# Performance work log

Hardware: AMD Instinct MI355X
Metric: run time of the kernel (lower is better)

## Reference

```python
import jax, jax.numpy as jnp
import numpy as np

B, D, K, E = 256, 256, 1024, 16  # batch, dim_codes, book_size, embedding_dim
DECAY = 0.999
GAIN = 1.0 - DECAY
EPS = 1e-6


def setup_inputs() -> dict:
    key = jax.random.key(0)
    k1, k2 = jax.random.split(key)
    return {
        "cw_q": jax.random.normal(k1, (B, D * E), dtype=jnp.float32),
        "codebook": jax.random.normal(k2, (D, K, E), dtype=jnp.float32),
        "ema_counts": jnp.ones((D, K), dtype=jnp.float32),
    }


def reference(cw_q, codebook, ema_counts):
    batch = cw_q.shape[0]
    x = cw_q.reshape(batch, D, E)  # [B, D, E]

    x2 = jnp.sum(x * x, axis=-1)                       # [B, D]
    c2 = jnp.sum(codebook * codebook, axis=-1)         # [D, K]
    xc = jnp.einsum('bde,dke->bdk', x, codebook)       # [B, D, K]
    dist = x2[:, :, None] + c2[None, :, :] - 2.0 * xc

    idx = jnp.argmin(dist, axis=-1)                    # [B, D] int32

    # gather nearest code vector per (batch, dim_code)
    cw_embed = codebook[jnp.arange(D)[None, :], idx]   # [B, D, E]
    cw_embed = cw_embed.reshape(batch, D * E)

    one_hot_idx = jax.nn.one_hot(idx, K, dtype=cw_q.dtype)  # [B, D, K]

    # EMA update (training path): scatter-sum of assigned vectors per code
    update = jnp.einsum('bdk,bde->dke', one_hot_idx, x)      # [D, K, E]
    new_codebook = codebook * DECAY + GAIN * update / (ema_counts[:, :, None] + EPS)
    new_ema_counts = DECAY * ema_counts + GAIN * jnp.sum(one_hot_idx, axis=0)

    return cw_embed, one_hot_idx, new_codebook, new_ema_counts
```

## Files before the change

### kernel.cpp

```cpp
#include <hip/hip_runtime.h>
#include <float.h>

#define BB 256
#define DD 256
#define KK 1024
#define EE 16
#define DECAY 0.999f
#define GAIN  0.001f
#define EPS   1e-6f

#define OH_OFF   ((size_t)BB * DD * EE)
#define CB_OFF   (OH_OFF + (size_t)BB * DD * KK)
#define EMA_OFF  (CB_OFF + (size_t)DD * KK * EE)

__device__ __forceinline__ float dot16(const float4& a0, const float4& a1,
                                       const float4& a2, const float4& a3,
                                       const float4& b0, const float4& b1,
                                       const float4& b2, const float4& b3) {
  float s = a0.x * b0.x;
  s = fmaf(a0.y, b0.y, s); s = fmaf(a0.z, b0.z, s); s = fmaf(a0.w, b0.w, s);
  s = fmaf(a1.x, b1.x, s); s = fmaf(a1.y, b1.y, s); s = fmaf(a1.z, b1.z, s); s = fmaf(a1.w, b1.w, s);
  s = fmaf(a2.x, b2.x, s); s = fmaf(a2.y, b2.y, s); s = fmaf(a2.z, b2.z, s); s = fmaf(a2.w, b2.w, s);
  s = fmaf(a3.x, b3.x, s); s = fmaf(a3.y, b3.y, s); s = fmaf(a3.z, b3.z, s); s = fmaf(a3.w, b3.w, s);
  return s;
}

__global__ __launch_bounds__(256, 2) void vq_assign(
    const float* __restrict__ cw_q,
    const float* __restrict__ codebook,
    float* __restrict__ out,
    int* __restrict__ idx_ws)
{
  __shared__ float4 cb4s[KK * EE / 4];
  __shared__ float  c2s[KK];
  __shared__ float  pbest[4 * 128];
  __shared__ int    pidxs[4 * 128];

  const int t  = threadIdx.x;
  const int d  = blockIdx.x >> 1;
  const int hf = blockIdx.x & 1;
  const int w  = t >> 6;
  const int l  = t & 63;

  const int b0 = hf * 128 + l;
  const int b1 = b0 + 64;
  const float4* xr0 = (const float4*)cw_q + (size_t)b0 * (DD * EE / 4) + d * 4;
  const float4* xr1 = (const float4*)cw_q + (size_t)b1 * (DD * EE / 4) + d * 4;
  float4 xa0 = xr0[0], xb0 = xr0[1], xc0 = xr0[2], xd0 = xr0[3];
  float4 xa1 = xr1[0], xb1 = xr1[1], xc1 = xr1[2], xd1 = xr1[3];

  const float4* src4 = (const float4*)codebook + (size_t)d * (KK * EE / 4);
  #pragma unroll
  for (int i = 0; i < 16; ++i) {
    int i4 = i * 256 + t;
    float4 v = src4[i4];
    cb4s[i4] = v;
    float sq = v.x * v.x;
    sq = fmaf(v.y, v.y, sq);
    sq = fmaf(v.z, v.z, sq);
    sq = fmaf(v.w, v.w, sq);
    sq += __shfl_xor(sq, 1);
    sq += __shfl_xor(sq, 2);
    if ((t & 3) == 0) c2s[i4 >> 2] = sq;
  }
  __syncthreads();

  const float x2_0 = dot16(xa0, xb0, xc0, xd0, xa0, xb0, xc0, xd0);
  const float x2_1 = dot16(xa1, xb1, xc1, xd1, xa1, xb1, xc1, xd1);

  float best0 = FLT_MAX, best1 = FLT_MAX;
  int   bi0 = 0, bi1 = 0;
  const int kbase = w << 8;

  float2* zbase = (float2*)(out + OH_OFF + (size_t)(hf * 128) * (DD * KK)
                            + (size_t)d * KK + kbase) + l;

  #pragma unroll 2
  for (int s = 0; s < 256; ++s) {
    const int k = kbase + s;
    const float4* p = cb4s + (k << 2);
    float4 c0 = p[0], c1 = p[1], c2v = p[2], c3 = p[3];

    float dot0 = dot16(c0, c1, c2v, c3, xa0, xb0, xc0, xd0);
    float dot1 = dot16(c0, c1, c2v, c3, xa1, xb1, xc1, xd1);
    const float c2k = c2s[k];
    float d0 = fmaf(-2.f, dot0, x2_0 + c2k);
    float d1 = fmaf(-2.f, dot1, x2_1 + c2k);
    if (d0 < best0) { best0 = d0; bi0 = k; }
    if (d1 < best1) { best1 = d1; bi1 = k; }

    const int r  = s >> 1;
    const int hh = s & 1;
    zbase[(size_t)r * (DD * KK / 2) + hh * 64] = make_float2(0.f, 0.f);
  }

  pbest[w * 128 + l]      = best0;  pidxs[w * 128 + l]      = bi0;
  pbest[w * 128 + l + 64] = best1;  pidxs[w * 128 + l + 64] = bi1;
  __syncthreads();

  if (t < 128) {
    float bb = pbest[t];
    int   bi = pidxs[t];
    #pragma unroll
    for (int w2 = 1; w2 < 4; ++w2) {
      float e = pbest[w2 * 128 + t];
      int   ii = pidxs[w2 * 128 + t];
      if (e < bb) { bb = e; bi = ii; }
    }
    const int b = hf * 128 + t;

    float4* ce = (float4*)out + (size_t)b * (DD * EE / 4) + d * 4;
    const float4* cw = cb4s + (bi << 2);
    ce[0] = cw[0]; ce[1] = cw[1]; ce[2] = cw[2]; ce[3] = cw[3];

    out[OH_OFF + (size_t)b * (DD * KK) + (size_t)d * KK + bi] = 1.0f;

    idx_ws[d * BB + b] = bi;
  }
}

__global__ __launch_bounds__(256) void vq_update(
    const float* __restrict__ cw_q,
    const float* __restrict__ codebook,
    const float* __restrict__ ema,
    const int* __restrict__ idx_ws,
    float* __restrict__ out)
{
  __shared__ float upds[KK * EE];
  __shared__ float cnts[KK];
  __shared__ float esh[KK];
  __shared__ int   ish[BB];

  const int t = threadIdx.x;
  const int d = blockIdx.x;
  float4* upd4 = (float4*)upds;
  const float4 z4 = make_float4(0.f, 0.f, 0.f, 0.f);

  #pragma unroll
  for (int i = 0; i < 16; ++i) upd4[i * 256 + t] = z4;
  #pragma unroll
  for (int j = 0; j < 4; ++j) cnts[t + 256 * j] = 0.f;
  __syncthreads();

  {
    int kidx = idx_ws[d * BB + t];
    ish[t] = kidx;
    atomicAdd(&cnts[kidx], 1.0f);
  }
  __syncthreads();

  {
    const int e = t & 15;
    const int g = t >> 4;
    #pragma unroll
    for (int i = 0; i < 16; ++i) {
      int b = g * 16 + i;
      int k = ish[b];
      float xv = cw_q[(size_t)b * (DD * EE) + (size_t)d * EE + e];
      atomicAdd(&upds[k * EE + e], xv);
    }
  }
  __syncthreads();

  const float* emad = ema + (size_t)d * KK;
  float* out_ema    = out + EMA_OFF + (size_t)d * KK;
  #pragma unroll
  for (int j = 0; j < 4; ++j) {
    int k = t + 256 * j;
    float ev = emad[k];
    esh[k] = ev;
    out_ema[k] = DECAY * ev + GAIN * cnts[k];
  }
  __syncthreads();

  const float4* cb4 = (const float4*)codebook + (size_t)d * (KK * EE / 4);
  float4* ocb4      = (float4*)(out + CB_OFF) + (size_t)d * (KK * EE / 4);
  #pragma unroll
  for (int i = 0; i < 16; ++i) {
    int i4 = i * 256 + t;
    int k  = i4 >> 2;
    float4 c = cb4[i4];
    float4 u = upd4[i4];
    float inv = GAIN / (esh[k] + EPS);
    float4 r;
    r.x = DECAY * c.x + u.x * inv;
    r.y = DECAY * c.y + u.y * inv;
    r.z = DECAY * c.z + u.z * inv;
    r.w = DECAY * c.w + u.w * inv;
    ocb4[i4] = r;
  }
}

extern "C" void kernel_launch(void* const* d_in, const int* in_sizes, int n_in,
                              void* d_out, int out_size, void* d_ws, size_t ws_size,
                              hipStream_t stream) {
  const float* cw_q     = (const float*)d_in[0];
  const float* codebook = (const float*)d_in[1];
  const float* ema      = (const float*)d_in[2];
  float* out  = (float*)d_out;
  int* idx_ws = (int*)d_ws;
  (void)in_sizes; (void)n_in; (void)out_size; (void)ws_size;

  vq_assign<<<dim3(512), dim3(256), 0, stream>>>(cw_q, codebook, out, idx_ws);
  vq_update<<<dim3(256), dim3(256), 0, stream>>>(cw_q, codebook, ema, idx_ws, out);
}
```

Before: 327.5 us.

## Fuse VQ assignment and EMA update into one kernel per code dimension

Merges the assign and update kernels into a single 512-thread block per dimension. Each block now handles all 256 batch rows, four per thread, and keeps the codebook in LDS for the EMA update. This removes the index round-trip through workspace, the second codebook read and one launch. The one-hot zero fill moves from float2 to float4 stores over contiguous row segments. The cost is about 150 KB of LDS per block, which allows only one block per CU, and half as many blocks (256 instead of 512).

```diff
diff --git a/kernel.cpp b/kernel.cpp
--- a/kernel.cpp
+++ b/kernel.cpp
@@ -25,34 +25,35 @@
   return s;
 }
 
-__global__ __launch_bounds__(256, 2) void vq_assign(
+__global__ __launch_bounds__(512, 2) void vqvae_fused(
     const float* __restrict__ cw_q,
     const float* __restrict__ codebook,
-    float* __restrict__ out,
-    int* __restrict__ idx_ws)
+    const float* __restrict__ ema,
+    float* __restrict__ out)
 {
   __shared__ float4 cb4s[KK * EE / 4];
+  __shared__ float4 upd4s[KK * EE / 4];
   __shared__ float  c2s[KK];
-  __shared__ float  pbest[4 * 128];
-  __shared__ int    pidxs[4 * 128];
+  __shared__ float  cnts[KK];
+  __shared__ float  pbest[8 * 256];
+  __shared__ int    pidxs[8 * 256];
+  __shared__ int    ish[BB];
 
-  const int t  = threadIdx.x;
-  const int d  = blockIdx.x >> 1;
-  const int hf = blockIdx.x & 1;
-  const int w  = t >> 6;
-  const int l  = t & 63;
+  const int t = threadIdx.x;
+  const int d = blockIdx.x;
+  const int w = t >> 6;
+  const int l = t & 63;
+  const float4 z4 = make_float4(0.f, 0.f, 0.f, 0.f);
 
-  const int b0 = hf * 128 + l;
-  const int b1 = b0 + 64;
-  const float4* xr0 = (const float4*)cw_q + (size_t)b0 * (DD * EE / 4) + d * 4;
-  const float4* xr1 = (const float4*)cw_q + (size_t)b1 * (DD * EE / 4) + d * 4;
-  float4 xa0 = xr0[0], xb0 = xr0[1], xc0 = xr0[2], xd0 = xr0[3];
-  float4 xa1 = xr1[0], xb1 = xr1[1], xc1 = xr1[2], xd1 = xr1[3];
+  #pragma unroll
+  for (int j = 0; j < 2; ++j) cnts[t + 512 * j] = 0.f;
+  #pragma unroll
+  for (int i = 0; i < 8; ++i) upd4s[i * 512 + t] = z4;
 
   const float4* src4 = (const float4*)codebook + (size_t)d * (KK * EE / 4);
   #pragma unroll
-  for (int i = 0; i < 16; ++i) {
-    int i4 = i * 256 + t;
+  for (int i = 0; i < 8; ++i) {
+    int i4 = i * 512 + t;
     float4 v = src4[i4];
     cb4s[i4] = v;
     float sq = v.x * v.x;
@@ -63,131 +64,118 @@
     sq += __shfl_xor(sq, 2);
     if ((t & 3) == 0) c2s[i4 >> 2] = sq;
   }
+
+  float4 xv[4][4];
+  float  x2[4];
+  #pragma unroll
+  for (int j = 0; j < 4; ++j) {
+    const int b = l + 64 * j;
+    const float4* xr = (const float4*)cw_q + (size_t)b * (DD * EE / 4) + d * 4;
+    xv[j][0] = xr[0]; xv[j][1] = xr[1]; xv[j][2] = xr[2]; xv[j][3] = xr[3];
+  }
   __syncthreads();
 
-  const float x2_0 = dot16(xa0, xb0, xc0, xd0, xa0, xb0, xc0, xd0);
-  const float x2_1 = dot16(xa1, xb1, xc1, xd1, xa1, xb1, xc1, xd1);
+  #pragma unroll
+  for (int j = 0; j < 4; ++j)
+    x2[j] = dot16(xv[j][0], xv[j][1], xv[j][2], xv[j][3],
+                  xv[j][0], xv[j][1], xv[j][2], xv[j][3]);
 
-  float best0 = FLT_MAX, best1 = FLT_MAX;
-  int   bi0 = 0, bi1 = 0;
-  const int kbase = w << 8;
+  float best[4] = {FLT_MAX, FLT_MAX, FLT_MAX, FLT_MAX};
+  int   bi[4]   = {0, 0, 0, 0};
+  const int kbase = w << 7;
 
-  float2* zbase = (float2*)(out + OH_OFF + (size_t)(hf * 128) * (DD * KK)
-                            + (size_t)d * KK + kbase) + l;
+  float* ohp = out + OH_OFF;
+  float4* zb = (float4*)(ohp + (size_t)(w << 5) * (DD * KK) + (size_t)d * KK) + l;
 
   #pragma unroll 2
-  for (int s = 0; s < 256; ++s) {
+  for (int s = 0; s < 128; ++s) {
     const int k = kbase + s;
     const float4* p = cb4s + (k << 2);
     float4 c0 = p[0], c1 = p[1], c2v = p[2], c3 = p[3];
+    const float c2k = c2s[k];
 
-    float dot0 = dot16(c0, c1, c2v, c3, xa0, xb0, xc0, xd0);
-    float dot1 = dot16(c0, c1, c2v, c3, xa1, xb1, xc1, xd1);
-    const float c2k = c2s[k];
-    float d0 = fmaf(-2.f, dot0, x2_0 + c2k);
-    float d1 = fmaf(-2.f, dot1, x2_1 + c2k);
-    if (d0 < best0) { best0 = d0; bi0 = k; }
-    if (d1 < best1) { best1 = d1; bi1 = k; }
+    #pragma unroll
+    for (int j = 0; j < 4; ++j) {
+      float dj = dot16(c0, c1, c2v, c3, xv[j][0], xv[j][1], xv[j][2], xv[j][3]);
+      float dist = fmaf(-2.f, dj, x2[j] + c2k);
+      if (dist < best[j]) { best[j] = dist; bi[j] = k; }
+    }
 
-    const int r  = s >> 1;
-    const int hh = s & 1;
-    zbase[(size_t)r * (DD * KK / 2) + hh * 64] = make_float2(0.f, 0.f);
+    zb[(size_t)(s >> 2) * (DD * KK / 4) + (s & 3) * 64] = z4;
   }
 
-  pbest[w * 128 + l]      = best0;  pidxs[w * 128 + l]      = bi0;
-  pbest[w * 128 + l + 64] = best1;  pidxs[w * 128 + l + 64] = bi1;
+  #pragma unroll
+  for (int j = 0; j < 4; ++j) {
+    pbest[w * 256 + l + 64 * j] = best[j];
+    pidxs[w * 256 + l + 64 * j] = bi[j];
+  }
   __syncthreads();
 
-  if (t < 128) {
-    float bb = pbest[t];
-    int   bi = pidxs[t];
+  if (t < 256) {
+    const int b = t;
+    float bb = pbest[b];
+    int   bidx = pidxs[b];
     #pragma unroll
-    for (int w2 = 1; w2 < 4; ++w2) {
-      float e = pbest[w2 * 128 + t];
-      int   ii = pidxs[w2 * 128 + t];
-      if (e < bb) { bb = e; bi = ii; }
+    for (int w2 = 1; w2 < 8; ++w2) {
+      float e = pbest[w2 * 256 + b];
+      int   ii = pidxs[w2 * 256 + b];
+      if (e < bb) { bb = e; bidx = ii; }
     }
-    const int b = hf * 128 + t;
 
     float4* ce = (float4*)out + (size_t)b * (DD * EE / 4) + d * 4;
-    const float4* cw = cb4s + (bi << 2);
-    ce[0] = cw[0]; ce[1] = cw[1]; ce[2] = cw[2]; ce[3] = cw[3];
+    const float4* cwp = cb4s + (bidx << 2);
+    ce[0] = cwp[0]; ce[1] = cwp[1]; ce[2] = cwp[2]; ce[3] = cwp[3];
 
-    out[OH_OFF + (size_t)b * (DD * KK) + (size_t)d * KK + bi] = 1.0f;
+    ohp[(size_t)b * (DD * KK) + (size_t)d * KK + bidx] = 1.0f;
 
-    idx_ws[d * BB + b] = bi;
-  }
-}
-
-__global__ __launch_bounds__(256) void vq_update(
-    const float* __restrict__ cw_q,
-    const float* __restrict__ codebook,
-    const float* __restrict__ ema,
-    const int* __restrict__ idx_ws,
-    float* __restrict__ out)
-{
-  __shared__ float upds[KK * EE];
-  __shared__ float cnts[KK];
-  __shared__ float esh[KK];
-  __shared__ int   ish[BB];
-
-  const int t = threadIdx.x;
-  const int d = blockIdx.x;
-  float4* upd4 = (float4*)upds;
-  const float4 z4 = make_float4(0.f, 0.f, 0.f, 0.f);
-
-  #pragma unroll
-  for (int i = 0; i < 16; ++i) upd4[i * 256 + t] = z4;
-  #pragma unroll
-  for (int j = 0; j < 4; ++j) cnts[t + 256 * j] = 0.f;
-  __syncthreads();
-
-  {
-    int kidx = idx_ws[d * BB + t];
-    ish[t] = kidx;
-    atomicAdd(&cnts[kidx], 1.0f);
+    ish[b] = bidx;
+    atomicAdd(&cnts[bidx], 1.0f);
   }
   __syncthreads();
 
   {
+    float* upd = (float*)upd4s;
     const int e = t & 15;
     const int g = t >> 4;
     #pragma unroll
-    for (int i = 0; i < 16; ++i) {
-      int b = g * 16 + i;
+    for (int i = 0; i < 8; ++i) {
+      int b = g * 8 + i;
       int k = ish[b];
-      float xv = cw_q[(size_t)b * (DD * EE) + (size_t)d * EE + e];
-      atomicAdd(&upds[k * EE + e], xv);
+      float xvv = cw_q[(size_t)b * (DD * EE) + (size_t)d * EE + e];
+      atomicAdd(&upd[k * EE + e], xvv);
     }
   }
   __syncthreads();
 
-  const float* emad = ema + (size_t)d * KK;
-  float* out_ema    = out + EMA_OFF + (size_t)d * KK;
-  #pragma unroll
-  for (int j = 0; j < 4; ++j) {
-    int k = t + 256 * j;
-    float ev = emad[k];
-    esh[k] = ev;
-    out_ema[k] = DECAY * ev + GAIN * cnts[k];
+  {
+    const float* emad = ema + (size_t)d * KK;
+    float* oe = out + EMA_OFF + (size_t)d * KK;
+    #pragma unroll
+    for (int j = 0; j < 2; ++j) {
+      int k = t + 512 * j;
+      float ev = emad[k];
+      c2s[k] = ev;
+      oe[k] = DECAY * ev + GAIN * cnts[k];
+    }
   }
   __syncthreads();
 
-  const float4* cb4 = (const float4*)codebook + (size_t)d * (KK * EE / 4);
-  float4* ocb4      = (float4*)(out + CB_OFF) + (size_t)d * (KK * EE / 4);
-  #pragma unroll
-  for (int i = 0; i < 16; ++i) {
-    int i4 = i * 256 + t;
-    int k  = i4 >> 2;
-    float4 c = cb4[i4];
-    float4 u = upd4[i4];
-    float inv = GAIN / (esh[k] + EPS);
-    float4 r;
-    r.x = DECAY * c.x + u.x * inv;
-    r.y = DECAY * c.y + u.y * inv;
-    r.z = DECAY * c.z + u.z * inv;
-    r.w = DECAY * c.w + u.w * inv;
-    ocb4[i4] = r;
+  {
+    float4* ocb = (float4*)(out + CB_OFF) + (size_t)d * (KK * EE / 4);
+    #pragma unroll
+    for (int i = 0; i < 8; ++i) {
+      int i4 = i * 512 + t;
+      int k  = i4 >> 2;
+      float4 c = cb4s[i4];
+      float4 u = upd4s[i4];
+      float inv = GAIN / (c2s[k] + EPS);
+      float4 r;
+      r.x = DECAY * c.x + u.x * inv;
+      r.y = DECAY * c.y + u.y * inv;
+      r.z = DECAY * c.z + u.z * inv;
+      r.w = DECAY * c.w + u.w * inv;
+      ocb[i4] = r;
+    }
   }
 }
 
@@ -197,10 +185,8 @@
   const float* cw_q     = (const float*)d_in[0];
   const float* codebook = (const float*)d_in[1];
   const float* ema      = (const float*)d_in[2];
-  float* out  = (float*)d_out;
-  int* idx_ws = (int*)d_ws;
-  (void)in_sizes; (void)n_in; (void)out_size; (void)ws_size;
+  float* out = (float*)d_out;
+  (void)in_sizes; (void)n_in; (void)out_size; (void)d_ws; (void)ws_size;
 
-  vq_assign<<<dim3(512), dim3(256), 0, stream>>>(cw_q, codebook, out, idx_ws);
-  vq_update<<<dim3(256), dim3(256), 0, stream>>>(cw_q, codebook, ema, idx_ws, out);
+  vqvae_fused<<<dim3(DD), dim3(512), 0, stream>>>(cw_q, codebook, ema, out);
 }
```

After: 326.1 us (median of 2 runs). Within noise of the previous version (-0.4%).
